# Optimization experiments

Hardware: AMD Instinct MI355X
Metric: run time of the kernel (lower is better)

The kernel has to match this reference:

```python
import jax, jax.numpy as jnp
import numpy as np

N, E, F_IN, H, C_OUT, G, L = 50000, 400000, 128, 128, 10, 512, 3
EPS = 1e-5
BN_BIAS = 1e-4  # BatchNorm1d weights init to 1, biases to 1e-4 in the source


def batchnorm(x):
    # training-mode BN, gamma=1, beta=1e-4 (as initialized in the module)
    m = x.mean(0)
    v = jnp.mean((x - m) ** 2, 0)
    return (x - m) * jax.lax.rsqrt(v + EPS) + BN_BIAS


def gcn_conv(x, W, b, src, dst, edge_weight=None):
    """CAL-style GCNConv: x@W, add self loops (weight 1), sym deg^-1/2 norm, scatter-add to dst."""
    n = x.shape[0]
    h = x @ W
    ew = jnp.ones(src.shape[0], x.dtype) if edge_weight is None else edge_weight
    loop = jnp.arange(n)
    row = jnp.concatenate([src, loop])
    col = jnp.concatenate([dst, loop])
    ew = jnp.concatenate([ew, jnp.ones(n, x.dtype)])
    deg = jax.ops.segment_sum(ew, row, num_segments=n)
    dis = jax.lax.rsqrt(jnp.where(deg > 0, deg, 1.0)) * (deg > 0)
    norm = dis[row] * ew * dis[col]
    out = jax.ops.segment_sum(norm[:, None] * h[row], col, num_segments=n)
    return out + b


def setup_inputs():
    key = jax.random.key(0)
    ks = jax.random.split(key, 32)
    rn = lambda k, shp, s=0.1: jax.random.normal(k, shp, jnp.float32) * s
    src = jax.random.randint(ks[0], (E,), 0, N, jnp.int32)
    dst = jax.random.randint(ks[1], (E,), 0, N, jnp.int32)
    dst = jnp.where(dst == src, (dst + 1) % N, dst)  # no self loops in data edges
    batch = jnp.sort(jax.random.randint(ks[2], (N,), 0, G, jnp.int32))
    return {
        'x': jax.random.normal(ks[3], (N, F_IN), jnp.float32),
        'W_feat': rn(ks[4], (F_IN, H)),
        'conv_Ws': rn(ks[5], (L, H, H)), 'conv_bs': rn(ks[6], (L, H), 0.01),
        'eW': rn(ks[7], (2 * H, 2)), 'eb': rn(ks[8], (2,), 0.01),
        'naW': rn(ks[9], (H, 2)), 'nab': rn(ks[10], (2,), 0.01),
        'xcW': rn(ks[11], (H, H)), 'xcb': rn(ks[12], (H,), 0.01),
        'xoW': rn(ks[13], (H, H)), 'xob': rn(ks[14], (H,), 0.01),
        'cW1': rn(ks[15], (H, H)), 'cb1': rn(ks[16], (H,), 0.01),
        'cW2': rn(ks[17], (H, C_OUT)), 'cb2': rn(ks[18], (C_OUT,), 0.01),
        'oW1': rn(ks[19], (H, H)), 'ob1': rn(ks[20], (H,), 0.01),
        'oW2': rn(ks[21], (H, C_OUT)), 'ob2': rn(ks[22], (C_OUT,), 0.01),
        'coW1': rn(ks[23], (2 * H, H)), 'cob1': rn(ks[24], (H,), 0.01),
        'coW2': rn(ks[25], (H, C_OUT)), 'cob2': rn(ks[26], (C_OUT,), 0.01),
        'edge_src': src, 'edge_dst': dst, 'batch': batch,
    }


def _forward(x, W_feat, conv_Ws, conv_bs, eW, eb, naW, nab, xcW, xcb, xoW, xob,
             cW1, cb1, cW2, cb2, oW1, ob1, oW2, ob2, coW1, cob1, coW2, cob2,
             edge_src, edge_dst, batch):
    # BIG: BN -> gfn conv (linear, no bias, no propagate) -> [BN -> GCNConv -> relu] x L
    h = batchnorm(x)
    h = jax.nn.relu(h @ W_feat)
    for i in range(L):
        h = batchnorm(h)
        h = jax.nn.relu(gcn_conv(h, conv_Ws[i], conv_bs[i], edge_src, edge_dst))
    # Att_cov: per-edge MLP softmax + per-node GCNConv softmax (shared by XC/XO)
    edge_rep = jnp.concatenate([h[edge_src], h[edge_dst]], axis=-1)  # [E, 2H]
    edge_att = jax.nn.softmax(edge_rep @ eW + eb, axis=-1)           # [E, 2]
    node_att = jax.nn.softmax(gcn_conv(h, naW, nab, edge_src, edge_dst), axis=-1)  # [N, 2]
    # XC branch (channel 0)
    xc = node_att[:, 0:1] * h
    xc = jax.nn.elu(gcn_conv(batchnorm(xc), xcW, xcb, edge_src, edge_dst, edge_att[:, 0]))
    xc = jax.ops.segment_sum(xc, batch, num_segments=G)  # global_add_pool [G, H]
    # XO branch (channel 1)
    xo = node_att[:, 1:2] * h
    xo = jax.nn.elu(gcn_conv(batchnorm(xo), xoW, xob, edge_src, edge_dst, edge_att[:, 1]))
    xo = jax.ops.segment_sum(xo, batch, num_segments=G)
    # C head
    c = batchnorm(xc)
    c = jax.nn.relu(c @ cW1 + cb1)
    c = batchnorm(c)
    c = jax.nn.log_softmax(c @ cW2 + cb2, axis=-1)
    # O head (Dropout1d inactive in eval)
    o = batchnorm(xo)
    o = jax.nn.relu(o @ oW1 + ob1)
    o = batchnorm(o)
    o = jax.nn.log_softmax(o @ oW2 + ob2, axis=-1)
    # CO head (cat branch; eval_random=False -> identity permutation); note elu applied twice
    co = jnp.concatenate([xc, xo], axis=1)
    co = batchnorm(co)
    co = jax.nn.elu(jax.nn.elu(co @ coW1 + cob1))
    co = batchnorm(co)
    co = jax.nn.log_softmax(co @ coW2 + cob2, axis=-1)
    return c, o, co


def reference(x, W_feat, conv_Ws, conv_bs, eW, eb, naW, nab, xcW, xcb, xoW, xob,
              cW1, cb1, cW2, cb2, oW1, ob1, oW2, ob2, coW1, cob1, coW2, cob2,
              edge_src, edge_dst, batch):
    return _forward(x, W_feat, conv_Ws, conv_bs, eW, eb, naW, nab, xcW, xcb, xoW, xob,
                    cW1, cb1, cW2, cb2, oW1, ob1, oW2, ob2, coW1, cob1, coW2, cob2,
                    edge_src, edge_dst, batch)
```

## Files before the change

### kernel.cpp

```cpp
#include <hip/hip_runtime.h>


typedef unsigned short bf16_t;
typedef unsigned int   uint32;
typedef __attribute__((ext_vector_type(8))) short   bf16x8;
typedef __attribute__((ext_vector_type(4))) float   f32x4;

#define CHNK 64

__device__ __forceinline__ float b2f(bf16_t v){ return __uint_as_float(((uint32)v) << 16); }
__device__ __forceinline__ bf16_t f2b(float f){
    uint32 u = __float_as_uint(f);
    return (bf16_t)((u + 0x7fffu + ((u >> 16) & 1u)) >> 16);
}
__device__ __forceinline__ uint32 pack2(float lo, float hi){
    return (uint32)f2b(lo) | ((uint32)f2b(hi) << 16);
}
__device__ __forceinline__ float lo16(uint32 u){ return __uint_as_float(u << 16); }
__device__ __forceinline__ float hi16(uint32 u){ return __uint_as_float(u & 0xffff0000u); }
__device__ __forceinline__ int   rl (int v, int l){ return __builtin_amdgcn_readlane(v, l); }
__device__ __forceinline__ float rlf(float v, int l){
    return __int_as_float(__builtin_amdgcn_readlane(__float_as_int(v), l));
}

__global__ void k_prologue(const float* __restrict__ Wf, const float* __restrict__ cWs,
        const float* __restrict__ xcW, const float* __restrict__ xoW,
        bf16_t* __restrict__ whiT, bf16_t* __restrict__ wloT,
        const int* __restrict__ esrc, const int* __restrict__ edst,
        uint32* __restrict__ cntD16, uint32* __restrict__ cntS16,
        int* __restrict__ rankE, int* __restrict__ rankS, int e,
        const float* __restrict__ x, float* __restrict__ st, int n, int WD)
{
    __shared__ uint32 h[12544];
    int bx = blockIdx.x, tid = threadIdx.x;
    if (bx < 256){
        int side = bx >> 7;
        int sub = bx & 127;
        int c = sub >> 1, hh = sub & 1;
        int Nh = ((n + 3) / 4) * 2;
        int lo = hh ? Nh : 0;
        int hi = hh ? n : Nh;
        int w0 = lo >> 1;
        int nw = (hi - lo + 1) >> 1;
        for (int j = tid; j < nw; j += 256) h[j] = 0;
        __syncthreads();
        int EC = (e + CHNK - 1) / CHNK;
        int beg = c * EC, endE = min(e, beg + EC);
        const int* keys = side ? esrc : edst;
        int* rank = side ? rankS : rankE;
        for (int i = beg + tid; i < endE; i += 256){
            int d = keys[i];
            if (d >= lo && d < hi){
                int w = (d >> 1) - w0;
                int sh = (d & 1) * 16;
                uint32 old = atomicAdd(&h[w], 1u << sh);
                rank[i] = (int)((old >> sh) & 0xffffu);
            }
        }
        __syncthreads();
        uint32* table = side ? cntS16 : cntD16;
        for (int j = tid; j < nw; j += 256)
            table[(size_t)c * WD + w0 + j] = h[j];
    } else if (bx < 352){
        int ms = bx - 256;
        int mat = ms >> 4, sub = ms & 15;
        const float* src = (mat == 0) ? Wf : (mat <= 3) ? cWs + (size_t)(mat - 1) * 16384
                          : (mat == 4) ? xcW : xoW;
        int i = (sub * 256 + tid) * 4;
        int nrow = i >> 7, k0 = i & 127;
        size_t off = (size_t)mat * 16384 + (size_t)nrow * 128 + k0;
        #pragma unroll
        for (int j = 0; j < 4; ++j){
            float w = src[(size_t)(k0 + j) * 128 + nrow];
            bf16_t hb = f2b(w);
            whiT[off + j] = hb;
            wloT[off + j] = f2b(w - b2f(hb));
        }
    } else {
        int bb = bx - 352;
        float* red = (float*)h;
        int f4 = (tid & 31) * 4, slice = tid >> 5;
        float s[4] = {0,0,0,0}, q[4] = {0,0,0,0};
        for (int row = bb * 8 + slice; row < n; row += 2048){
            float4 v = *(const float4*)&x[(size_t)row * 128 + f4];
            s[0]+=v.x; q[0]+=v.x*v.x; s[1]+=v.y; q[1]+=v.y*v.y;
            s[2]+=v.z; q[2]+=v.z*v.z; s[3]+=v.w; q[3]+=v.w*v.w;
        }
        #pragma unroll
        for (int j = 0; j < 4; ++j){
            red[slice * 128 + f4 + j] = s[j];
            red[1024 + slice * 128 + f4 + j] = q[j];
        }
        __syncthreads();
        if (tid < 128){
            float ts=0.f, tq=0.f;
            #pragma unroll
            for (int w = 0; w < 8; ++w){ ts += red[w*128+tid]; tq += red[1024+w*128+tid]; }
            atomicAdd(&st[tid], ts); atomicAdd(&st[128+tid], tq);
        }
    }
}

__global__ void k_chunkscan(uint32* __restrict__ cntD16, uint32* __restrict__ cntS16,
        int* __restrict__ cntI, float* __restrict__ degUf, int WD, int n)
{
    int g = blockIdx.x * 256 + threadIdx.x;
    if (g >= 2 * WD) return;
    int side = (g >= WD);
    int w = side ? g - WD : g;
    uint32* tab = side ? cntS16 : cntD16;
    uint32 r0 = 0, r1 = 0;
    for (int c = 0; c < CHNK; ++c){
        size_t idx = (size_t)c * WD + w;
        uint32 v = tab[idx];
        tab[idx] = r0 | (r1 << 16);
        r0 += v & 0xffffu; r1 += v >> 16;
    }
    int b0 = 2 * w, b1 = 2 * w + 1;
    if (!side){
        if (b0 < n) cntI[b0] = (int)r0;
        if (b1 < n) cntI[b1] = (int)r1;
    } else {
        if (b0 < n){ cntI[n + b0] = (int)r0; degUf[b0] = (float)r0; }
        if (b1 < n){ cntI[n + b1] = (int)r1; degUf[b1] = (float)r1; }
    }
}

__global__ __launch_bounds__(256) void k_statsB(const bf16_t* __restrict__ a,
        float* __restrict__ st, int n){
    __shared__ float red[2][16][128];
    int tid = threadIdx.x;
    int c8 = (tid & 15) * 8, slice = tid >> 4;
    float s[8] = {0,0,0,0,0,0,0,0}, q[8] = {0,0,0,0,0,0,0,0};
    for (int row = blockIdx.x * 16 + slice; row < n; row += 4096){
        uint4 v = *(const uint4*)&a[(size_t)row * 128 + c8];
        const bf16_t* pv = (const bf16_t*)&v;
        #pragma unroll
        for (int j = 0; j < 8; ++j){ float f = b2f(pv[j]); s[j] += f; q[j] += f * f; }
    }
    #pragma unroll
    for (int j = 0; j < 8; ++j){ red[0][slice][c8+j]=s[j]; red[1][slice][c8+j]=q[j]; }
    __syncthreads();
    if (tid < 128){
        float ts=0.f, tq=0.f;
        #pragma unroll
        for (int w = 0; w < 16; ++w){ ts += red[0][w][tid]; tq += red[1][w][tid]; }
        atomicAdd(&st[tid], ts); atomicAdd(&st[128+tid], tq);
    }
}

template<int ACT, int INBF>
__global__ __launch_bounds__(256, 3) void k_gemm(const void* __restrict__ Av,
        const float* __restrict__ scale, int sch,
        const float* __restrict__ st, const bf16_t* __restrict__ WhiT,
        const bf16_t* __restrict__ WloT,
        bf16_t* __restrict__ C, int ldc, int ccol0, int n)
{
    __shared__ bf16_t As[64 * 136];
    __shared__ bf16_t Whi[128 * 72];
    __shared__ bf16_t Wlo[128 * 72];
    int tid = threadIdx.x;
    int wid = tid >> 6, lane = tid & 63;
    int row0 = blockIdx.x * 64;
    int m0 = wid * 16;
    int q8 = (lane >> 4) * 8, l15 = lane & 15;

    int c8t = (tid & 15) * 8;
    float sM[8], sR[8];
    #pragma unroll
    for (int j = 0; j < 8; ++j){
        float m = st[c8t + j] / n;
        float var = st[128 + c8t + j] / n - m * m;
        sM[j] = m; sR[j] = rsqrtf(var + 1e-5f);
    }

    for (int i = tid; i < 64 * 16; i += 256){
        int r = i >> 4, c8 = (i & 15) * 8;
        int gr = row0 + r;
        float v[8];
        if (gr < n){
            float sc = scale ? scale[(size_t)gr * 2 + sch] : 1.f;
            if (INBF){
                const bf16_t* Ab = (const bf16_t*)Av;
                ushort4 qa = *(const ushort4*)&Ab[(size_t)gr * 128 + c8];
                ushort4 qb = *(const ushort4*)&Ab[(size_t)gr * 128 + c8 + 4];
                v[0]=b2f(qa.x); v[1]=b2f(qa.y); v[2]=b2f(qa.z); v[3]=b2f(qa.w);
                v[4]=b2f(qb.x); v[5]=b2f(qb.y); v[6]=b2f(qb.z); v[7]=b2f(qb.w);
            } else {
                const float* Af = (const float*)Av;
                float4 fa = *(const float4*)&Af[(size_t)gr * 128 + c8];
                float4 fb = *(const float4*)&Af[(size_t)gr * 128 + c8 + 4];
                v[0]=fa.x; v[1]=fa.y; v[2]=fa.z; v[3]=fa.w;
                v[4]=fb.x; v[5]=fb.y; v[6]=fb.z; v[7]=fb.w;
            }
            #pragma unroll
            for (int j = 0; j < 8; ++j)
                v[j] = (v[j] * sc - sM[j]) * sR[j] + 1e-4f;
        } else {
            #pragma unroll
            for (int j = 0; j < 8; ++j) v[j] = 0.f;
        }
        #pragma unroll
        for (int j = 0; j < 8; ++j) As[r * 136 + c8 + j] = f2b(v[j]);
    }

    f32x4 acc[8];
    #pragma unroll
    for (int t = 0; t < 8; ++t) acc[t] = (f32x4){0.f, 0.f, 0.f, 0.f};

    for (int kc = 0; kc < 128; kc += 64){
        __syncthreads();
        for (int i = tid; i < 128 * 8; i += 256){
            int nrow = i >> 3, k8 = (i & 7) * 8;
            *(uint4*)&Whi[nrow * 72 + k8] = *(const uint4*)&WhiT[(size_t)nrow * 128 + kc + k8];
            *(uint4*)&Wlo[nrow * 72 + k8] = *(const uint4*)&WloT[(size_t)nrow * 128 + kc + k8];
        }
        __syncthreads();
        #pragma unroll
        for (int kbl = 0; kbl < 2; ++kbl){
            bf16x8 a = *(const bf16x8*)&As[(m0 + l15) * 136 + kc + kbl * 32 + q8];
            #pragma unroll
            for (int nt = 0; nt < 8; ++nt){
                bf16x8 bh = *(const bf16x8*)&Whi[(nt * 16 + l15) * 72 + kbl * 32 + q8];
                acc[nt] = __builtin_amdgcn_mfma_f32_16x16x32_bf16(a, bh, acc[nt], 0, 0, 0);
                bf16x8 bl = *(const bf16x8*)&Wlo[(nt * 16 + l15) * 72 + kbl * 32 + q8];
                acc[nt] = __builtin_amdgcn_mfma_f32_16x16x32_bf16(a, bl, acc[nt], 0, 0, 0);
            }
        }
    }

    __syncthreads();
    #pragma unroll
    for (int nt = 0; nt < 8; ++nt){
        #pragma unroll
        for (int r = 0; r < 4; ++r){
            float v = acc[nt][r];
            if (ACT == 1) v = fmaxf(v, 0.f);
            As[(m0 + (lane >> 4) * 4 + r) * 136 + nt * 16 + l15] = f2b(v);
        }
    }
    __syncthreads();
    for (int i = tid; i < 64 * 16; i += 256){
        int r = i >> 4, c8 = (i & 15) * 8;
        int gr = row0 + r;
        if (gr < n)
            *(uint4*)&C[(size_t)gr * ldc + ccol0 + c8] = *(const uint4*)&As[r * 136 + c8];
    }
}

__global__ __launch_bounds__(256, 3) void k_gemm2(const bf16_t* __restrict__ Ab,
        const float* __restrict__ natt, const float* __restrict__ stBase,
        const bf16_t* __restrict__ whiT6, const bf16_t* __restrict__ wloT6,
        bf16_t* __restrict__ C, int n)
{
    __shared__ bf16_t As[64 * 136];
    __shared__ bf16_t Whi[128 * 72];
    __shared__ bf16_t Wlo[128 * 72];
    int brn = blockIdx.y;
    const float* st = stBase + brn * 256;
    const bf16_t* WhiT = whiT6 + (size_t)(4 + brn) * 16384;
    const bf16_t* WloT = wloT6 + (size_t)(4 + brn) * 16384;
    int ccol0 = brn * 128;
    const int ldc = 256;

    int tid = threadIdx.x;
    int wid = tid >> 6, lane = tid & 63;
    int row0 = blockIdx.x * 64;
    int m0 = wid * 16;
    int q8 = (lane >> 4) * 8, l15 = lane & 15;

    int c8t = (tid & 15) * 8;
    float sM[8], sR[8];
    #pragma unroll
    for (int j = 0; j < 8; ++j){
        float m = st[c8t + j] / n;
        float var = st[128 + c8t + j] / n - m * m;
        sM[j] = m; sR[j] = rsqrtf(var + 1e-5f);
    }

    for (int i = tid; i < 64 * 16; i += 256){
        int r = i >> 4, c8 = (i & 15) * 8;
        int gr = row0 + r;
        float v[8];
        if (gr < n){
            float sc = natt[(size_t)gr * 2 + brn];
            ushort4 qa = *(const ushort4*)&Ab[(size_t)gr * 128 + c8];
            ushort4 qb = *(const ushort4*)&Ab[(size_t)gr * 128 + c8 + 4];
            v[0]=b2f(qa.x); v[1]=b2f(qa.y); v[2]=b2f(qa.z); v[3]=b2f(qa.w);
            v[4]=b2f(qb.x); v[5]=b2f(qb.y); v[6]=b2f(qb.z); v[7]=b2f(qb.w);
            #pragma unroll
            for (int j = 0; j < 8; ++j)
                v[j] = (v[j] * sc - sM[j]) * sR[j] + 1e-4f;
        } else {
            #pragma unroll
            for (int j = 0; j < 8; ++j) v[j] = 0.f;
        }
        #pragma unroll
        for (int j = 0; j < 8; ++j) As[r * 136 + c8 + j] = f2b(v[j]);
    }

    f32x4 acc[8];
    #pragma unroll
    for (int t = 0; t < 8; ++t) acc[t] = (f32x4){0.f, 0.f, 0.f, 0.f};

    for (int kc = 0; kc < 128; kc += 64){
        __syncthreads();
        for (int i = tid; i < 128 * 8; i += 256){
            int nrow = i >> 3, k8 = (i & 7) * 8;
            *(uint4*)&Whi[nrow * 72 + k8] = *(const uint4*)&WhiT[(size_t)nrow * 128 + kc + k8];
            *(uint4*)&Wlo[nrow * 72 + k8] = *(const uint4*)&WloT[(size_t)nrow * 128 + kc + k8];
        }
        __syncthreads();
        #pragma unroll
        for (int kbl = 0; kbl < 2; ++kbl){
            bf16x8 a = *(const bf16x8*)&As[(m0 + l15) * 136 + kc + kbl * 32 + q8];
            #pragma unroll
            for (int nt = 0; nt < 8; ++nt){
                bf16x8 bh = *(const bf16x8*)&Whi[(nt * 16 + l15) * 72 + kbl * 32 + q8];
                acc[nt] = __builtin_amdgcn_mfma_f32_16x16x32_bf16(a, bh, acc[nt], 0, 0, 0);
                bf16x8 bl = *(const bf16x8*)&Wlo[(nt * 16 + l15) * 72 + kbl * 32 + q8];
                acc[nt] = __builtin_amdgcn_mfma_f32_16x16x32_bf16(a, bl, acc[nt], 0, 0, 0);
            }
        }
    }

    __syncthreads();
    #pragma unroll
    for (int nt = 0; nt < 8; ++nt){
        #pragma unroll
        for (int r = 0; r < 4; ++r){
            As[(m0 + (lane >> 4) * 4 + r) * 136 + nt * 16 + l15] = f2b(acc[nt][r]);
        }
    }
    __syncthreads();
    for (int i = tid; i < 64 * 16; i += 256){
        int r = i >> 4, c8 = (i & 15) * 8;
        int gr = row0 + r;
        if (gr < n)
            *(uint4*)&C[(size_t)gr * ldc + ccol0 + c8] = *(const uint4*)&As[r * 136 + c8];
    }
}

__global__ __launch_bounds__(1024) void k_scanA(const int* __restrict__ cnt,
        int* __restrict__ ptr, int* __restrict__ bsum, int n){
    __shared__ int wsum[16];
    int t = threadIdx.x, lane = t & 63, wid = t >> 6;
    int i = blockIdx.x * 1024 + t;
    int v = (i < n) ? cnt[i] : 0;
    int s = v;
    for (int off = 1; off < 64; off <<= 1){
        int u = __shfl_up(s, off);
        if (lane >= off) s += u;
    }
    if (lane == 63) wsum[wid] = s;
    __syncthreads();
    if (wid == 0 && lane < 16){
        int ws = wsum[lane];
        for (int off = 1; off < 16; off <<= 1){
            int u = __shfl_up(ws, off);
            if (lane >= off) ws += u;
        }
        wsum[lane] = ws;
    }
    __syncthreads();
    int woff = wid ? wsum[wid - 1] : 0;
    if (i < n) ptr[i] = woff + s - v;
    if (t == 1023) bsum[blockIdx.x] = woff + s;
}
__global__ void k_scanB(int* __restrict__ bsum, int* __restrict__ ptrN, int nb){
    int lane = threadIdx.x;
    int carry = 0;
    for (int base = 0; base < nb; base += 64){
        int i = base + lane;
        int v = (i < nb) ? bsum[i] : 0;
        int s = v;
        for (int off = 1; off < 64; off <<= 1){
            int u = __shfl_up(s, off);
            if (lane >= off) s += u;
        }
        if (i < nb) bsum[i] = carry + s - v;
        carry += __shfl(s, 63);
    }
    if (lane == 0) *ptrN = carry;
}
__global__ __launch_bounds__(1024) void k_scanC(int* __restrict__ ptr,
        const int* __restrict__ bsum, int n){
    int i = blockIdx.x * 1024 + threadIdx.x;
    if (i < n) ptr[i] += bsum[blockIdx.x];
}
__global__ void k_fill(const int* __restrict__ esrc, const int* __restrict__ edst,
        const int* __restrict__ rankE, const int* __restrict__ rankS,
        const uint32* __restrict__ cntD16, const uint32* __restrict__ cntS16,
        const int* __restrict__ ptr, const float* __restrict__ degUf,
        int* __restrict__ srcC, int* __restrict__ dstC, int* __restrict__ dstS,
        float* __restrict__ wU, int e, int n, int WD, int EC)
{
    int i = blockIdx.x * 256 + threadIdx.x;
    if (i >= e) return;
    int s = esrc[i], d = edst[i];
    int c = i / EC;
    uint32 pw = cntD16[(size_t)c * WD + (d >> 1)];
    int offD = (d & 1) ? (int)(pw >> 16) : (int)(pw & 0xffffu);
    int dslot = ptr[d] + offD + rankE[i];
    uint32 sw = cntS16[(size_t)c * WD + (s >> 1)];
    int offS = (s & 1) ? (int)(sw >> 16) : (int)(sw & 0xffffu);
    int sslot = (ptr[n + s] - e) + offS + rankS[i];
    srcC[dslot] = s;
    dstC[dslot] = d;
    wU[dslot] = rsqrtf(degUf[s] + 1.0f);
    dstS[sslot] = d;
}

template<int PREP>
__global__ __launch_bounds__(256) void k_gather0(const int* __restrict__ ptr,
        const int* __restrict__ srcC, const float* __restrict__ wE,
        const float* __restrict__ degU, const bf16_t* __restrict__ t,
        const float* __restrict__ bias, bf16_t* __restrict__ outB,
        const float* __restrict__ eW, const float* __restrict__ naW,
        float4* __restrict__ epre, float* __restrict__ ntT, int n, int nwaves)
{
    int wid = blockIdx.x * 4 + (threadIdx.x >> 6);
    int lane = threadIdx.x & 63;
    const uint32* T = (const uint32*)t;
    float bias0 = bias[2 * lane], bias1 = bias[2 * lane + 1];
    for (int node = wid; node < n; node += nwaves){
        float dd = rsqrtf(degU[node] + 1.0f);
        uint32 sv = T[(size_t)node * 64 + lane];
        float a0 = 0.f, a1 = 0.f;
        int k = ptr[node], end = ptr[node + 1];
        while (k < end){
            int cnt = min(end - k, 64);
            int kl = k + min(lane, cnt - 1);
            int   myI = srcC[kl];
            float myW = wE[kl];
            int j = 0;
            for (; j + 8 <= cnt; j += 8){
                int s0 = rl(myI, j),     s1 = rl(myI, j + 1), s2 = rl(myI, j + 2), s3 = rl(myI, j + 3);
                int s4 = rl(myI, j + 4), s5 = rl(myI, j + 5), s6 = rl(myI, j + 6), s7 = rl(myI, j + 7);
                float w0 = rlf(myW, j),     w1 = rlf(myW, j + 1), w2 = rlf(myW, j + 2), w3 = rlf(myW, j + 3);
                float w4 = rlf(myW, j + 4), w5 = rlf(myW, j + 5), w6 = rlf(myW, j + 6), w7 = rlf(myW, j + 7);
                uint32 v0 = T[(size_t)s0 * 64 + lane];
                uint32 v1 = T[(size_t)s1 * 64 + lane];
                uint32 v2 = T[(size_t)s2 * 64 + lane];
                uint32 v3 = T[(size_t)s3 * 64 + lane];
                uint32 v4 = T[(size_t)s4 * 64 + lane];
                uint32 v5 = T[(size_t)s5 * 64 + lane];
                uint32 v6 = T[(size_t)s6 * 64 + lane];
                uint32 v7 = T[(size_t)s7 * 64 + lane];
                a0 += w0 * lo16(v0) + w1 * lo16(v1) + w2 * lo16(v2) + w3 * lo16(v3);
                a1 += w0 * hi16(v0) + w1 * hi16(v1) + w2 * hi16(v2) + w3 * hi16(v3);
                a0 += w4 * lo16(v4) + w5 * lo16(v5) + w6 * lo16(v6) + w7 * lo16(v7);
                a1 += w4 * hi16(v4) + w5 * hi16(v5) + w6 * hi16(v6) + w7 * hi16(v7);
            }
            for (; j < cnt; ++j){
                int s = rl(myI, j);
                float w = rlf(myW, j);
                uint32 v = T[(size_t)s * 64 + lane];
                a0 += w * lo16(v); a1 += w * hi16(v);
            }
            k += cnt;
        }
        a0 = fmaxf(dd * (a0 + dd * lo16(sv)) + bias0, 0.f);
        a1 = fmaxf(dd * (a1 + dd * hi16(sv)) + bias1, 0.f);
        ((uint32*)outB)[(size_t)node * 64 + lane] = pack2(a0, a1);
        if (PREP){
            float s0 = a0 * eW[4 * lane]           + a1 * eW[4 * lane + 2];
            float s1 = a0 * eW[4 * lane + 1]       + a1 * eW[4 * lane + 3];
            float d0 = a0 * eW[256 + 4 * lane]     + a1 * eW[256 + 4 * lane + 2];
            float d1 = a0 * eW[256 + 4 * lane + 1] + a1 * eW[256 + 4 * lane + 3];
            float n0 = a0 * naW[4 * lane]          + a1 * naW[4 * lane + 2];
            float n1 = a0 * naW[4 * lane + 1]      + a1 * naW[4 * lane + 3];
            for (int off = 32; off; off >>= 1){
                s0 += __shfl_xor(s0, off); s1 += __shfl_xor(s1, off);
                d0 += __shfl_xor(d0, off); d1 += __shfl_xor(d1, off);
                n0 += __shfl_xor(n0, off); n1 += __shfl_xor(n1, off);
            }
            if (lane == 0){
                epre[node] = make_float4(s0, s1, d0, d1);
                ntT[2 * node] = n0; ntT[2 * node + 1] = n1;
            }
        }
    }
}

__global__ __launch_bounds__(256) void k_gatherP2(const int* __restrict__ ptr,
        const int* __restrict__ srcC, const float* __restrict__ w0E,
        const float* __restrict__ w1E, const float* __restrict__ degC0,
        const float* __restrict__ degU, const bf16_t* __restrict__ t,
        const float* __restrict__ biasC, const float* __restrict__ biasO,
        const int* __restrict__ batch, float* __restrict__ pool0,
        float* __restrict__ pool1, int n, int span, int nwb)
{
    int br  = blockIdx.x & 1;
    int wvb = (blockIdx.x >> 1) * 4 + (threadIdx.x >> 6);
    int lane = threadIdx.x & 63;
    const float* wE   = br ? w1E : w0E;
    const float* bias = br ? biasO : biasC;
    float* pool       = br ? pool1 : pool0;
    float b0 = bias[2 * lane], b1 = bias[2 * lane + 1];
    const uint32* T = (const uint32*)t;
    int rowoff = (br ? 64 : 0) + lane;
    int nspans = (n + span - 1) / span;
    for (int sp = wvb; sp < nspans; sp += nwb){
        int nbeg = sp * span;
        int nend = min(n, nbeg + span);
        int curG = -1;
        float p0 = 0.f, p1 = 0.f;
        for (int node = nbeg; node < nend; ++node){
            float d0v = degC0[node];
            float dv  = br ? (degU[node] - d0v) : d0v;
            float dd  = rsqrtf(dv + 1.0f);
            uint32 sv = T[(size_t)node * 128 + rowoff];
            float a0 = 0.f, a1 = 0.f;
            int k = ptr[node], end = ptr[node + 1];
            while (k < end){
                int cnt = min(end - k, 64);
                int kl = k + min(lane, cnt - 1);
                int   myI = srcC[kl];
                float myW = wE[kl];
                int j = 0;
                for (; j + 8 <= cnt; j += 8){
                    int s0 = rl(myI, j),     s1 = rl(myI, j + 1), s2 = rl(myI, j + 2), s3 = rl(myI, j + 3);
                    int s4 = rl(myI, j + 4), s5 = rl(myI, j + 5), s6 = rl(myI, j + 6), s7 = rl(myI, j + 7);
                    float w0 = rlf(myW, j),     w1 = rlf(myW, j + 1), w2 = rlf(myW, j + 2), w3 = rlf(myW, j + 3);
                    float w4 = rlf(myW, j + 4), w5 = rlf(myW, j + 5), w6 = rlf(myW, j + 6), w7 = rlf(myW, j + 7);
                    uint32 v0 = T[(size_t)s0 * 128 + rowoff];
                    uint32 v1 = T[(size_t)s1 * 128 + rowoff];
                    uint32 v2 = T[(size_t)s2 * 128 + rowoff];
                    uint32 v3 = T[(size_t)s3 * 128 + rowoff];
                    uint32 v4 = T[(size_t)s4 * 128 + rowoff];
                    uint32 v5 = T[(size_t)s5 * 128 + rowoff];
                    uint32 v6 = T[(size_t)s6 * 128 + rowoff];
                    uint32 v7 = T[(size_t)s7 * 128 + rowoff];
                    a0 += w0 * lo16(v0) + w1 * lo16(v1) + w2 * lo16(v2) + w3 * lo16(v3);
                    a1 += w0 * hi16(v0) + w1 * hi16(v1) + w2 * hi16(v2) + w3 * hi16(v3);
                    a0 += w4 * lo16(v4) + w5 * lo16(v5) + w6 * lo16(v6) + w7 * lo16(v7);
                    a1 += w4 * hi16(v4) + w5 * hi16(v5) + w6 * hi16(v6) + w7 * hi16(v7);
                }
                for (; j < cnt; ++j){
                    int s = rl(myI, j);
                    float w = rlf(myW, j);
                    uint32 v = T[(size_t)s * 128 + rowoff];
                    a0 += w * lo16(v); a1 += w * hi16(v);
                }
                k += cnt;
            }
            a0 = dd * (a0 + dd * lo16(sv)) + b0;
            a1 = dd * (a1 + dd * hi16(sv)) + b1;
            a0 = a0 > 0.f ? a0 : expm1f(a0);
            a1 = a1 > 0.f ? a1 : expm1f(a1);
            int g = batch[node];
            if (g != curG){
                if (curG >= 0){
                    float* p = pool + (size_t)curG * 128 + 2 * lane;
                    atomicAdd(&p[0], p0); atomicAdd(&p[1], p1);
                }
                curG = g; p0 = a0; p1 = a1;
            } else {
                p0 += a0; p1 += a1;
            }
        }
        if (curG >= 0){
            float* p = pool + (size_t)curG * 128 + 2 * lane;
            atomicAdd(&p[0], p0); atomicAdd(&p[1], p1);
        }
    }
}

__global__ void k_eattnatt(const int* __restrict__ srcC, const int* __restrict__ dstC,
        const int* __restrict__ dstS,
        const float4* __restrict__ epre, const float* __restrict__ eb,
        float* __restrict__ wB0, float* __restrict__ wB1,
        float* __restrict__ degC0,
        const int* __restrict__ ptr, const float* __restrict__ wU,
        const float* __restrict__ degU, const float* __restrict__ ntT,
        const float* __restrict__ nab, float* __restrict__ natt,
        int e, int n, int gridN, int gridE)
{
    int bx = blockIdx.x;
    if (bx < gridN){
        int i = bx * 256 + threadIdx.x;
        if (i >= n) return;
        float dd = rsqrtf(degU[i] + 1.0f);
        float z0 = 0.f, z1 = 0.f;
        int end = ptr[i + 1];
        for (int k = ptr[i]; k < end; ++k){
            int s = srcC[k];
            float w = wU[k];
            z0 += w * ntT[2 * s]; z1 += w * ntT[2 * s + 1];
        }
        z0 = dd * (z0 + dd * ntT[2 * i])     + nab[0];
        z1 = dd * (z1 + dd * ntT[2 * i + 1]) + nab[1];
        float m = fmaxf(z0, z1);
        float e0 = expf(z0 - m), e1 = expf(z1 - m);
        float inv = 1.f / (e0 + e1);
        natt[2 * i] = e0 * inv; natt[2 * i + 1] = e1 * inv;
    } else if (bx < gridN + gridE){
        int i = (bx - gridN) * 256 + threadIdx.x;
        if (i >= e) return;
        int s = srcC[i];
        float4 ps = epre[s], pd = epre[dstC[i]];
        float l0 = ps.x + pd.z + eb[0], l1 = ps.y + pd.w + eb[1];
        float m = fmaxf(l0, l1);
        float e0 = expf(l0 - m), e1 = expf(l1 - m);
        float inv = 1.f / (e0 + e1);
        wB0[i] = e0 * inv; wB1[i] = e1 * inv;
    } else {
        int s = (bx - gridN - gridE) * 256 + threadIdx.x;
        if (s >= n) return;
        float4 ps = epre[s];
        float eb0 = eb[0], eb1 = eb[1];
        int beg = ptr[n + s] - e, endk = ptr[n + s + 1] - e;
        float sum = 0.f;
        for (int k = beg; k < endk; ++k){
            int d = dstS[k];
            float4 pd = epre[d];
            float l0 = ps.x + pd.z + eb0, l1 = ps.y + pd.w + eb1;
            float m = fmaxf(l0, l1);
            float e0 = expf(l0 - m), e1v = expf(l1 - m);
            sum += e0 / (e0 + e1v);
        }
        degC0[s] = sum;
    }
}

__global__ void k_stats2wB(const bf16_t* __restrict__ a, const float* __restrict__ natt,
        float* __restrict__ st, int n,
        const int* __restrict__ srcC, const float* __restrict__ degC0,
        const float* __restrict__ degU, float* __restrict__ w0,
        float* __restrict__ w1, int e)
{
    __shared__ float red[2][16][128];
    int bx = blockIdx.x, tid = threadIdx.x;
    if (bx < 256){
        int c8 = (tid & 15) * 8, slice = tid >> 4;
        float s0[8]={0,0,0,0,0,0,0,0}, q0[8]={0,0,0,0,0,0,0,0};
        float s1[8]={0,0,0,0,0,0,0,0}, q1[8]={0,0,0,0,0,0,0,0};
        for (int row = bx * 16 + slice; row < n; row += 4096){
            uint4 v = *(const uint4*)&a[(size_t)row * 128 + c8];
            const bf16_t* pv = (const bf16_t*)&v;
            float2 w = *(const float2*)&natt[(size_t)row * 2];
            #pragma unroll
            for (int j = 0; j < 8; ++j){
                float f = b2f(pv[j]);
                float f0 = f * w.x, f1 = f * w.y;
                s0[j] += f0; q0[j] += f0 * f0;
                s1[j] += f1; q1[j] += f1 * f1;
            }
        }
        #pragma unroll
        for (int j = 0; j < 8; ++j){ red[0][slice][c8+j]=s0[j]; red[1][slice][c8+j]=q0[j]; }
        __syncthreads();
        if (tid < 128){
            float ts=0.f, tq=0.f;
            #pragma unroll
            for (int w = 0; w < 16; ++w){ ts += red[0][w][tid]; tq += red[1][w][tid]; }
            atomicAdd(&st[tid], ts); atomicAdd(&st[128+tid], tq);
        }
        __syncthreads();
        #pragma unroll
        for (int j = 0; j < 8; ++j){ red[0][slice][c8+j]=s1[j]; red[1][slice][c8+j]=q1[j]; }
        __syncthreads();
        if (tid < 128){
            float ts=0.f, tq=0.f;
            #pragma unroll
            for (int w = 0; w < 16; ++w){ ts += red[0][w][tid]; tq += red[1][w][tid]; }
            atomicAdd(&st[256+tid], ts); atomicAdd(&st[384+tid], tq);
        }
    } else {
        int i = (bx - 256) * 256 + tid;
        if (i < e){
            int s = srcC[i];
            float d0v = degC0[s];
            w0[i] *= rsqrtf(d0v + 1.0f);
            w1[i] *= rsqrtf(degU[s] - d0v + 1.0f);
        }
    }
}

__global__ __launch_bounds__(1024) void k_gstats3(const float* __restrict__ xcp,
        const float* __restrict__ xop, float* __restrict__ mrsH, int n){
    __shared__ float red[2][1024];
    int head = blockIdx.x;
    const float* a = (head == 1) ? xop : xcp;
    const float* b = (head == 0) ? xcp : xop;
    int f = (head == 2) ? 256 : 128;
    float* mrs = mrsH + head * 512;
    int col = threadIdx.x & (f - 1);
    int rpb = 1024 / f;
    int rw  = threadIdx.x / f;
    float s = 0.f, sq = 0.f;
    for (int r = rw; r < n; r += rpb){
        float v = (col < 128) ? a[(size_t)r * 128 + col] : b[(size_t)r * 128 + col - 128];
        s += v; sq += v * v;
    }
    red[0][threadIdx.x] = s; red[1][threadIdx.x] = sq;
    __syncthreads();
    if (threadIdx.x < (unsigned)f){
        float ts = 0.f, tq = 0.f;
        for (int w = 0; w < rpb; ++w){ ts += red[0][w * f + col]; tq += red[1][w * f + col]; }
        float m = ts / n, var = tq / n - m * m;
        mrs[col] = m; mrs[f + col] = rsqrtf(var + 1e-5f);
    }
}
__global__ __launch_bounds__(128) void k_hgemm3(const float* __restrict__ xcp,
        const float* __restrict__ xop, const float* __restrict__ mrsH,
        const float* __restrict__ cW1, const float* __restrict__ cb1,
        const float* __restrict__ oW1, const float* __restrict__ ob1,
        const float* __restrict__ coW1, const float* __restrict__ cob1,
        float* __restrict__ gt3)
{
    __shared__ float as[256];
    int head = blockIdx.y, row = blockIdx.x, tid = threadIdx.x;
    const float* a  = (head == 1) ? xop : xcp;
    const float* b2 = (head == 0) ? xcp : xop;
    int fin = (head == 2) ? 256 : 128;
    const float* mrs = mrsH + head * 512;
    const float* W  = (head == 0) ? cW1 : (head == 1) ? oW1 : coW1;
    const float* bb = (head == 0) ? cb1 : (head == 1) ? ob1 : cob1;
    float* o = gt3 + (size_t)head * 512 * 128;
    for (int i = tid; i < fin; i += 128){
        float v = (i < 128) ? a[(size_t)row * 128 + i] : b2[(size_t)row * 128 + i - 128];
        as[i] = (v - mrs[i]) * mrs[fin + i] + 1e-4f;
    }
    __syncthreads();
    float s = 0.f;
    for (int k = 0; k < fin; ++k) s += as[k] * W[k * 128 + tid];
    s += bb[tid];
    if (head < 2) s = fmaxf(s, 0.f);
    else { s = s > 0.f ? s : expm1f(s); s = s > 0.f ? s : expm1f(s); }
    o[(size_t)row * 128 + tid] = s;
}
__global__ __launch_bounds__(1024) void k_gstats3b(const float* __restrict__ gt3,
        float* __restrict__ mrsH2, int n){
    __shared__ float red[2][1024];
    int head = blockIdx.x;
    const float* a = gt3 + (size_t)head * 512 * 128;
    float* mrs = mrsH2 + head * 256;
    int col = threadIdx.x & 127;
    int rw  = threadIdx.x >> 7;
    float s = 0.f, sq = 0.f;
    for (int r = rw; r < n; r += 8){
        float v = a[(size_t)r * 128 + col];
        s += v; sq += v * v;
    }
    red[0][threadIdx.x] = s; red[1][threadIdx.x] = sq;
    __syncthreads();
    if (threadIdx.x < 128u){
        float ts = 0.f, tq = 0.f;
        for (int w = 0; w < 8; ++w){ ts += red[0][w * 128 + col]; tq += red[1][w * 128 + col]; }
        float m = ts / n, var = tq / n - m * m;
        mrs[col] = m; mrs[128 + col] = rsqrtf(var + 1e-5f);
    }
}
__global__ __launch_bounds__(256) void k_hfinal3(const float* __restrict__ gt3,
        const float* __restrict__ mrsH2,
        const float* __restrict__ cW2, const float* __restrict__ cb2,
        const float* __restrict__ oW2, const float* __restrict__ ob2,
        const float* __restrict__ coW2, const float* __restrict__ cob2,
        float* __restrict__ out, int nrows)
{
    int head = blockIdx.y;
    int row = blockIdx.x * 4 + (threadIdx.x >> 6);
    if (row >= nrows) return;
    int lane = threadIdx.x & 63;
    const float* a   = gt3 + (size_t)head * 512 * 128;
    const float* mrs = mrsH2 + head * 256;
    const float* W = (head == 0) ? cW2 : (head == 1) ? oW2 : coW2;
    const float* b = (head == 0) ? cb2 : (head == 1) ? ob2 : cob2;
    float* o = out + (size_t)head * nrows * 10;
    float v0 = (a[(size_t)row * 128 + lane]      - mrs[lane])      * mrs[128 + lane]      + 1e-4f;
    float v1 = (a[(size_t)row * 128 + 64 + lane] - mrs[64 + lane]) * mrs[128 + 64 + lane] + 1e-4f;
    float logit[10];
    #pragma unroll
    for (int c = 0; c < 10; ++c){
        float p = v0 * W[lane * 10 + c] + v1 * W[(lane + 64) * 10 + c];
        for (int off = 32; off; off >>= 1) p += __shfl_xor(p, off);
        logit[c] = p + b[c];
    }
    float m = logit[0];
    #pragma unroll
    for (int c = 1; c < 10; ++c) m = fmaxf(m, logit[c]);
    float s = 0.f;
    #pragma unroll
    for (int c = 0; c < 10; ++c) s += expf(logit[c] - m);
    float lse = logf(s);
    if (lane < 10) o[row * 10 + lane] = logit[lane] - m - lse;
}

extern "C" void kernel_launch(void* const* d_in, const int* in_sizes, int n_in,
                              void* d_out, int out_size, void* d_ws, size_t ws_size,
                              hipStream_t stream)
{
    const int N = in_sizes[0] / 128;
    const int E = in_sizes[24];
    const int G = 512;
    const float* x    = (const float*)d_in[0];
    const float* Wf   = (const float*)d_in[1];
    const float* cWs  = (const float*)d_in[2];
    const float* cbs  = (const float*)d_in[3];
    const float* eW   = (const float*)d_in[4];
    const float* ebv  = (const float*)d_in[5];
    const float* naW  = (const float*)d_in[6];
    const float* nab  = (const float*)d_in[7];
    const float* xcW  = (const float*)d_in[8];
    const float* xcb  = (const float*)d_in[9];
    const float* xoW  = (const float*)d_in[10];
    const float* xob  = (const float*)d_in[11];
    const float* cW1  = (const float*)d_in[12];
    const float* cb1  = (const float*)d_in[13];
    const float* cW2  = (const float*)d_in[14];
    const float* cb2  = (const float*)d_in[15];
    const float* oW1  = (const float*)d_in[16];
    const float* ob1  = (const float*)d_in[17];
    const float* oW2  = (const float*)d_in[18];
    const float* ob2  = (const float*)d_in[19];
    const float* coW1 = (const float*)d_in[20];
    const float* cob1 = (const float*)d_in[21];
    const float* coW2 = (const float*)d_in[22];
    const float* cob2 = (const float*)d_in[23];
    const int* esrc  = (const int*)d_in[24];
    const int* edst  = (const int*)d_in[25];
    const int* batch = (const int*)d_in[26];
    float* out = (float*)d_out;

    const int WD = (N + 1) / 2;
    const int EC = (E + CHNK - 1) / CHNK;

    size_t NH = (size_t)N * 128;
    bf16_t* B1  = (bf16_t*)d_ws;
    bf16_t* B0  = B1 + NH;
    bf16_t* B0c = B0 + NH;
    float* fbase = (float*)(B0c + 2 * NH);
    float* epreF = fbase;
    float* ntT   = epreF + 4 * (size_t)N;
    float* natt  = ntT + 2 * (size_t)N;
    float* mrsH  = natt + 2 * (size_t)N;
    float* mrsH2 = mrsH + 1536;
    float* wU    = mrsH2 + 768;
    float* wB0   = wU + E;
    float* wB1   = wB0 + E;
    float* gt3   = wB1 + E;
    float* degU  = gt3 + (size_t)3 * G * 128;
    float* degC0 = degU + N;
    float* stZ   = degC0 + N;
    float* xcp   = stZ + 1536;
    float* xop   = xcp + (size_t)G * 128;
    size_t zzBytes = (1536 + 2 * (size_t)G * 128) * 4;
    int* cntI   = (int*)(xop + (size_t)G * 128);
    int* ptrI   = cntI + 2 * N;
    int* srcC   = ptrI + 2 * N + 1;
    int* dstC   = srcC + E;
    int* dstS   = dstC + E;
    int* rankE  = dstS + E;
    int* rankS  = rankE + E;
    int* bsum   = rankS + E;
    uint32* cntD16 = (uint32*)(bsum + 128);
    uint32* cntS16 = cntD16 + (size_t)CHNK * WD;
    bf16_t* whiT = (bf16_t*)((((size_t)(cntS16 + (size_t)CHNK * WD)) + 15) & ~(size_t)15);
    bf16_t* wloT = whiT + 6 * 16384;
    float4* epre = (float4*)epreF;

    int gridE = (E + 255) / 256;
    int gridN = (N + 255) / 256;
    int gridG = (N + 63) / 64;
    int n2    = 2 * N;
    int nb2   = (n2 + 1023) / 1024;
    int gridCS = (2 * WD + 255) / 256;
    int span  = 4;
    const int PW_BLOCKS = 2048;
    const int NWAVES = PW_BLOCKS * 4;
    const int NWB = (PW_BLOCKS / 2) * 4;

    hipMemsetAsync(stZ, 0, zzBytes, stream);

    k_prologue<<<608, 256, 0, stream>>>(Wf, cWs, xcW, xoW, whiT, wloT,
            esrc, edst, cntD16, cntS16, rankE, rankS, E, x, stZ, N, WD);

    k_chunkscan<<<gridCS, 256, 0, stream>>>(cntD16, cntS16, cntI, degU, WD, N);
    k_scanA<<<nb2, 1024, 0, stream>>>(cntI, ptrI, bsum, n2);
    k_scanB<<<1, 64, 0, stream>>>(bsum, ptrI + n2, nb2);
    k_scanC<<<nb2, 1024, 0, stream>>>(ptrI, bsum, n2);
    k_fill<<<gridE, 256, 0, stream>>>(esrc, edst, rankE, rankS, cntD16, cntS16,
            ptrI, degU, srcC, dstC, dstS, wU, E, N, WD, EC);

    k_gemm<1, 0><<<gridG, 256, 0, stream>>>(x, nullptr, 0, stZ, whiT, wloT, B1, 128, 0, N);

    for (int i = 0; i < 3; ++i){
        float* st = stZ + 256 * (i + 1);
        k_statsB<<<256, 256, 0, stream>>>(B1, st, N);
        k_gemm<0, 1><<<gridG, 256, 0, stream>>>(B1, nullptr, 0, st,
                whiT + (size_t)(i + 1) * 16384, wloT + (size_t)(i + 1) * 16384,
                B0, 128, 0, N);
        if (i < 2)
            k_gather0<0><<<PW_BLOCKS, 256, 0, stream>>>(ptrI, srcC, wU, degU, B0,
                    cbs + i * 128, B1, eW, naW, epre, ntT, N, NWAVES);
        else
            k_gather0<1><<<PW_BLOCKS, 256, 0, stream>>>(ptrI, srcC, wU, degU, B0,
                    cbs + i * 128, B1, eW, naW, epre, ntT, N, NWAVES);
    }

    k_eattnatt<<<gridN + gridE + gridN, 256, 0, stream>>>(srcC, dstC, dstS, epre, ebv,
            wB0, wB1, degC0, ptrI, wU, degU, ntT, nab, natt, E, N, gridN, gridE);

    k_stats2wB<<<256 + gridE, 256, 0, stream>>>(B1, natt, stZ + 1024, N,
            srcC, degC0, degU, wB0, wB1, E);

    k_gemm2<<<dim3(gridG, 2), 256, 0, stream>>>(B1, natt, stZ + 1024, whiT, wloT, B0c, N);
    k_gatherP2<<<PW_BLOCKS, 256, 0, stream>>>(ptrI, srcC, wB0, wB1, degC0, degU, B0c,
                                              xcb, xob, batch, xcp, xop, N, span, NWB);

    k_gstats3<<<3, 1024, 0, stream>>>(xcp, xop, mrsH, G);
    k_hgemm3<<<dim3(G, 3), 128, 0, stream>>>(xcp, xop, mrsH, cW1, cb1, oW1, ob1,
                                             coW1, cob1, gt3);
    k_gstats3b<<<3, 1024, 0, stream>>>(gt3, mrsH2, G);
    k_hfinal3<<<dim3((G + 3) / 4, 3), 256, 0, stream>>>(gt3, mrsH2, cW2, cb2, oW2, ob2,
                                                        coW2, cob2, out, G);
}
```

Baseline: 549.2 us.

## Fuse BN stats into gather kernel and replace readlane edge broadcast with scalar loads

The batch-norm column sums and sums of squares for layers 2 and 3 are now accumulated inside the gather kernel and flushed with per-wave atomics, which removes two separate k_statsB passes over the 50000x128 activation buffer. The gather inner loops also drop the cooperative lane-load plus readlane broadcast of edge indices and weights in favour of direct uniform loads from srcC and wE, with 8-, 4- and 1-wide tails. The stats are computed in fp32 before the bf16 pack rather than from the stored bf16 values, so they can differ slightly. Atomics add some contention, with 8192 waves writing to 256 floats.

```diff
diff --git a/kernel.cpp b/kernel.cpp
--- a/kernel.cpp
+++ b/kernel.cpp
@@ -18,10 +18,6 @@
 }
 __device__ __forceinline__ float lo16(uint32 u){ return __uint_as_float(u << 16); }
 __device__ __forceinline__ float hi16(uint32 u){ return __uint_as_float(u & 0xffff0000u); }
-__device__ __forceinline__ int   rl (int v, int l){ return __builtin_amdgcn_readlane(v, l); }
-__device__ __forceinline__ float rlf(float v, int l){
-    return __int_as_float(__builtin_amdgcn_readlane(__float_as_int(v), l));
-}
 
 __global__ void k_prologue(const float* __restrict__ Wf, const float* __restrict__ cWs,
         const float* __restrict__ xcW, const float* __restrict__ xoW,
@@ -411,58 +407,66 @@
     dstS[sslot] = d;
 }
 
-template<int PREP>
+template<int PREP, int STATS>
 __global__ __launch_bounds__(256) void k_gather0(const int* __restrict__ ptr,
         const int* __restrict__ srcC, const float* __restrict__ wE,
         const float* __restrict__ degU, const bf16_t* __restrict__ t,
         const float* __restrict__ bias, bf16_t* __restrict__ outB,
         const float* __restrict__ eW, const float* __restrict__ naW,
-        float4* __restrict__ epre, float* __restrict__ ntT, int n, int nwaves)
-{
-    int wid = blockIdx.x * 4 + (threadIdx.x >> 6);
+        float4* __restrict__ epre, float* __restrict__ ntT,
+        float* __restrict__ stOut, int n, int nwaves)
+{
+    int wvid = blockIdx.x * 4 + (threadIdx.x >> 6);
     int lane = threadIdx.x & 63;
     const uint32* T = (const uint32*)t;
     float bias0 = bias[2 * lane], bias1 = bias[2 * lane + 1];
-    for (int node = wid; node < n; node += nwaves){
+    float ps0 = 0.f, pq0 = 0.f, ps1 = 0.f, pq1 = 0.f;
+    for (int node = wvid; node < n; node += nwaves){
         float dd = rsqrtf(degU[node] + 1.0f);
         uint32 sv = T[(size_t)node * 64 + lane];
         float a0 = 0.f, a1 = 0.f;
         int k = ptr[node], end = ptr[node + 1];
-        while (k < end){
-            int cnt = min(end - k, 64);
-            int kl = k + min(lane, cnt - 1);
-            int   myI = srcC[kl];
-            float myW = wE[kl];
-            int j = 0;
-            for (; j + 8 <= cnt; j += 8){
-                int s0 = rl(myI, j),     s1 = rl(myI, j + 1), s2 = rl(myI, j + 2), s3 = rl(myI, j + 3);
-                int s4 = rl(myI, j + 4), s5 = rl(myI, j + 5), s6 = rl(myI, j + 6), s7 = rl(myI, j + 7);
-                float w0 = rlf(myW, j),     w1 = rlf(myW, j + 1), w2 = rlf(myW, j + 2), w3 = rlf(myW, j + 3);
-                float w4 = rlf(myW, j + 4), w5 = rlf(myW, j + 5), w6 = rlf(myW, j + 6), w7 = rlf(myW, j + 7);
-                uint32 v0 = T[(size_t)s0 * 64 + lane];
-                uint32 v1 = T[(size_t)s1 * 64 + lane];
-                uint32 v2 = T[(size_t)s2 * 64 + lane];
-                uint32 v3 = T[(size_t)s3 * 64 + lane];
-                uint32 v4 = T[(size_t)s4 * 64 + lane];
-                uint32 v5 = T[(size_t)s5 * 64 + lane];
-                uint32 v6 = T[(size_t)s6 * 64 + lane];
-                uint32 v7 = T[(size_t)s7 * 64 + lane];
-                a0 += w0 * lo16(v0) + w1 * lo16(v1) + w2 * lo16(v2) + w3 * lo16(v3);
-                a1 += w0 * hi16(v0) + w1 * hi16(v1) + w2 * hi16(v2) + w3 * hi16(v3);
-                a0 += w4 * lo16(v4) + w5 * lo16(v5) + w6 * lo16(v6) + w7 * lo16(v7);
-                a1 += w4 * hi16(v4) + w5 * hi16(v5) + w6 * hi16(v6) + w7 * hi16(v7);
-            }
-            for (; j < cnt; ++j){
-                int s = rl(myI, j);
-                float w = rlf(myW, j);
-                uint32 v = T[(size_t)s * 64 + lane];
-                a0 += w * lo16(v); a1 += w * hi16(v);
-            }
-            k += cnt;
+        for (; k + 8 <= end; k += 8){
+            int s0 = srcC[k],     s1 = srcC[k + 1], s2 = srcC[k + 2], s3 = srcC[k + 3];
+            int s4 = srcC[k + 4], s5 = srcC[k + 5], s6 = srcC[k + 6], s7 = srcC[k + 7];
+            float w0 = wE[k],     w1 = wE[k + 1], w2 = wE[k + 2], w3 = wE[k + 3];
+            float w4 = wE[k + 4], w5 = wE[k + 5], w6 = wE[k + 6], w7 = wE[k + 7];
+            uint32 v0 = T[(size_t)s0 * 64 + lane];
+            uint32 v1 = T[(size_t)s1 * 64 + lane];
+            uint32 v2 = T[(size_t)s2 * 64 + lane];
+            uint32 v3 = T[(size_t)s3 * 64 + lane];
+            uint32 v4 = T[(size_t)s4 * 64 + lane];
+            uint32 v5 = T[(size_t)s5 * 64 + lane];
+            uint32 v6 = T[(size_t)s6 * 64 + lane];
+            uint32 v7 = T[(size_t)s7 * 64 + lane];
+            a0 += w0 * lo16(v0) + w1 * lo16(v1) + w2 * lo16(v2) + w3 * lo16(v3);
+            a1 += w0 * hi16(v0) + w1 * hi16(v1) + w2 * hi16(v2) + w3 * hi16(v3);
+            a0 += w4 * lo16(v4) + w5 * lo16(v5) + w6 * lo16(v6) + w7 * lo16(v7);
+            a1 += w4 * hi16(v4) + w5 * hi16(v5) + w6 * hi16(v6) + w7 * hi16(v7);
+        }
+        for (; k + 4 <= end; k += 4){
+            int s0 = srcC[k], s1 = srcC[k + 1], s2 = srcC[k + 2], s3 = srcC[k + 3];
+            float w0 = wE[k], w1 = wE[k + 1], w2 = wE[k + 2], w3 = wE[k + 3];
+            uint32 v0 = T[(size_t)s0 * 64 + lane];
+            uint32 v1 = T[(size_t)s1 * 64 + lane];
+            uint32 v2 = T[(size_t)s2 * 64 + lane];
+            uint32 v3 = T[(size_t)s3 * 64 + lane];
+            a0 += w0 * lo16(v0) + w1 * lo16(v1) + w2 * lo16(v2) + w3 * lo16(v3);
+            a1 += w0 * hi16(v0) + w1 * hi16(v1) + w2 * hi16(v2) + w3 * hi16(v3);
+        }
+        for (; k < end; ++k){
+            int s = srcC[k];
+            float w = wE[k];
+            uint32 v = T[(size_t)s * 64 + lane];
+            a0 += w * lo16(v); a1 += w * hi16(v);
         }
         a0 = fmaxf(dd * (a0 + dd * lo16(sv)) + bias0, 0.f);
         a1 = fmaxf(dd * (a1 + dd * hi16(sv)) + bias1, 0.f);
         ((uint32*)outB)[(size_t)node * 64 + lane] = pack2(a0, a1);
+        if (STATS){
+            ps0 += a0; pq0 += a0 * a0;
+            ps1 += a1; pq1 += a1 * a1;
+        }
         if (PREP){
             float s0 = a0 * eW[4 * lane]           + a1 * eW[4 * lane + 2];
             float s1 = a0 * eW[4 * lane + 1]       + a1 * eW[4 * lane + 3];
@@ -480,6 +484,12 @@
                 ntT[2 * node] = n0; ntT[2 * node + 1] = n1;
             }
         }
+    }
+    if (STATS){
+        atomicAdd(&stOut[2 * lane],       ps0);
+        atomicAdd(&stOut[2 * lane + 1],   ps1);
+        atomicAdd(&stOut[128 + 2 * lane], pq0);
+        atomicAdd(&stOut[129 + 2 * lane], pq1);
     }
 }
 
@@ -513,37 +523,39 @@
             uint32 sv = T[(size_t)node * 128 + rowoff];
             float a0 = 0.f, a1 = 0.f;
             int k = ptr[node], end = ptr[node + 1];
-            while (k < end){
-                int cnt = min(end - k, 64);
-                int kl = k + min(lane, cnt - 1);
-                int   myI = srcC[kl];
-                float myW = wE[kl];
-                int j = 0;
-                for (; j + 8 <= cnt; j += 8){
-                    int s0 = rl(myI, j),     s1 = rl(myI, j + 1), s2 = rl(myI, j + 2), s3 = rl(myI, j + 3);
-                    int s4 = rl(myI, j + 4), s5 = rl(myI, j + 5), s6 = rl(myI, j + 6), s7 = rl(myI, j + 7);
-                    float w0 = rlf(myW, j),     w1 = rlf(myW, j + 1), w2 = rlf(myW, j + 2), w3 = rlf(myW, j + 3);
-                    float w4 = rlf(myW, j + 4), w5 = rlf(myW, j + 5), w6 = rlf(myW, j + 6), w7 = rlf(myW, j + 7);
-                    uint32 v0 = T[(size_t)s0 * 128 + rowoff];
-                    uint32 v1 = T[(size_t)s1 * 128 + rowoff];
-                    uint32 v2 = T[(size_t)s2 * 128 + rowoff];
-                    uint32 v3 = T[(size_t)s3 * 128 + rowoff];
-                    uint32 v4 = T[(size_t)s4 * 128 + rowoff];
-                    uint32 v5 = T[(size_t)s5 * 128 + rowoff];
-                    uint32 v6 = T[(size_t)s6 * 128 + rowoff];
-                    uint32 v7 = T[(size_t)s7 * 128 + rowoff];
-                    a0 += w0 * lo16(v0) + w1 * lo16(v1) + w2 * lo16(v2) + w3 * lo16(v3);
-                    a1 += w0 * hi16(v0) + w1 * hi16(v1) + w2 * hi16(v2) + w3 * hi16(v3);
-                    a0 += w4 * lo16(v4) + w5 * lo16(v5) + w6 * lo16(v6) + w7 * lo16(v7);
-                    a1 += w4 * hi16(v4) + w5 * hi16(v5) + w6 * hi16(v6) + w7 * hi16(v7);
-                }
-                for (; j < cnt; ++j){
-                    int s = rl(myI, j);
-                    float w = rlf(myW, j);
-                    uint32 v = T[(size_t)s * 128 + rowoff];
-                    a0 += w * lo16(v); a1 += w * hi16(v);
-                }
-                k += cnt;
+            for (; k + 8 <= end; k += 8){
+                int s0 = srcC[k],     s1 = srcC[k + 1], s2 = srcC[k + 2], s3 = srcC[k + 3];
+                int s4 = srcC[k + 4], s5 = srcC[k + 5], s6 = srcC[k + 6], s7 = srcC[k + 7];
+                float w0 = wE[k],     w1 = wE[k + 1], w2 = wE[k + 2], w3 = wE[k + 3];
+                float w4 = wE[k + 4], w5 = wE[k + 5], w6 = wE[k + 6], w7 = wE[k + 7];
+                uint32 v0 = T[(size_t)s0 * 128 + rowoff];
+                uint32 v1 = T[(size_t)s1 * 128 + rowoff];
+                uint32 v2 = T[(size_t)s2 * 128 + rowoff];
+                uint32 v3 = T[(size_t)s3 * 128 + rowoff];
+                uint32 v4 = T[(size_t)s4 * 128 + rowoff];
+                uint32 v5 = T[(size_t)s5 * 128 + rowoff];
+                uint32 v6 = T[(size_t)s6 * 128 + rowoff];
+                uint32 v7 = T[(size_t)s7 * 128 + rowoff];
+                a0 += w0 * lo16(v0) + w1 * lo16(v1) + w2 * lo16(v2) + w3 * lo16(v3);
+                a1 += w0 * hi16(v0) + w1 * hi16(v1) + w2 * hi16(v2) + w3 * hi16(v3);
+                a0 += w4 * lo16(v4) + w5 * lo16(v5) + w6 * lo16(v6) + w7 * lo16(v7);
+                a1 += w4 * hi16(v4) + w5 * hi16(v5) + w6 * hi16(v6) + w7 * hi16(v7);
+            }
+            for (; k + 4 <= end; k += 4){
+                int s0 = srcC[k], s1 = srcC[k + 1], s2 = srcC[k + 2], s3 = srcC[k + 3];
+                float w0 = wE[k], w1 = wE[k + 1], w2 = wE[k + 2], w3 = wE[k + 3];
+                uint32 v0 = T[(size_t)s0 * 128 + rowoff];
+                uint32 v1 = T[(size_t)s1 * 128 + rowoff];
+                uint32 v2 = T[(size_t)s2 * 128 + rowoff];
+                uint32 v3 = T[(size_t)s3 * 128 + rowoff];
+                a0 += w0 * lo16(v0) + w1 * lo16(v1) + w2 * lo16(v2) + w3 * lo16(v3);
+                a1 += w0 * hi16(v0) + w1 * hi16(v1) + w2 * hi16(v2) + w3 * hi16(v3);
+            }
+            for (; k < end; ++k){
+                int s = srcC[k];
+                float w = wE[k];
+                uint32 v = T[(size_t)s * 128 + rowoff];
+                a0 += w * lo16(v); a1 += w * hi16(v);
             }
             a0 = dd * (a0 + dd * lo16(sv)) + b0;
             a1 = dd * (a1 + dd * hi16(sv)) + b1;
@@ -886,19 +898,19 @@
 
     k_gemm<1, 0><<<gridG, 256, 0, stream>>>(x, nullptr, 0, stZ, whiT, wloT, B1, 128, 0, N);
 
-    for (int i = 0; i < 3; ++i){
-        float* st = stZ + 256 * (i + 1);
-        k_statsB<<<256, 256, 0, stream>>>(B1, st, N);
-        k_gemm<0, 1><<<gridG, 256, 0, stream>>>(B1, nullptr, 0, st,
-                whiT + (size_t)(i + 1) * 16384, wloT + (size_t)(i + 1) * 16384,
-                B0, 128, 0, N);
-        if (i < 2)
-            k_gather0<0><<<PW_BLOCKS, 256, 0, stream>>>(ptrI, srcC, wU, degU, B0,
-                    cbs + i * 128, B1, eW, naW, epre, ntT, N, NWAVES);
-        else
-            k_gather0<1><<<PW_BLOCKS, 256, 0, stream>>>(ptrI, srcC, wU, degU, B0,
-                    cbs + i * 128, B1, eW, naW, epre, ntT, N, NWAVES);
-    }
+    k_statsB<<<256, 256, 0, stream>>>(B1, stZ + 256, N);
+    k_gemm<0, 1><<<gridG, 256, 0, stream>>>(B1, nullptr, 0, stZ + 256,
+            whiT + (size_t)1 * 16384, wloT + (size_t)1 * 16384, B0, 128, 0, N);
+    k_gather0<0, 1><<<PW_BLOCKS, 256, 0, stream>>>(ptrI, srcC, wU, degU, B0,
+            cbs + 0 * 128, B1, eW, naW, epre, ntT, stZ + 512, N, NWAVES);
+    k_gemm<0, 1><<<gridG, 256, 0, stream>>>(B1, nullptr, 0, stZ + 512,
+            whiT + (size_t)2 * 16384, wloT + (size_t)2 * 16384, B0, 128, 0, N);
+    k_gather0<0, 1><<<PW_BLOCKS, 256, 0, stream>>>(ptrI, srcC, wU, degU, B0,
+            cbs + 1 * 128, B1, eW, naW, epre, ntT, stZ + 768, N, NWAVES);
+    k_gemm<0, 1><<<gridG, 256, 0, stream>>>(B1, nullptr, 0, stZ + 768,
+            whiT + (size_t)3 * 16384, wloT + (size_t)3 * 16384, B0, 128, 0, N);
+    k_gather0<1, 0><<<PW_BLOCKS, 256, 0, stream>>>(ptrI, srcC, wU, degU, B0,
+            cbs + 2 * 128, B1, eW, naW, epre, ntT, nullptr, N, NWAVES);
 
     k_eattnatt<<<gridN + gridE + gridN, 256, 0, stream>>>(srcC, dstC, dstS, epre, ebv,
             wB0, wB1, degC0, ptrI, wU, degU, ntT, nab, natt, E, N, gridN, gridE);
```

Result: slower. 1.314 ms (+139.3%).
